# Optimization experiments

Hardware: AMD Instinct MI355X
Metric: run time of the kernel (lower is better)

The kernel has to match this reference:

```python
import jax, jax.numpy as jnp
import numpy as np

FACTOR = 27.2114 * 0.529177249  # Hartree*Bohr -> eV*Angstrom coulomb factor
N_TYPES = 6
NEURON = [25, 50, 100]
AXIS = 16
B, NC, NM = 4, 128, 16384


def _dense_stack(x, channels, params):
    """Type-indexed MLP: x (B,N,F), channels (N,) int -> (B,N,neuron[-1]).
    Layer 0: no residual; layers 1,2: out=2*in -> residual via concat([x,x])."""
    res_modes = [0, 2, 2]
    for (W, b), res in zip(params, res_modes):
        # W: (C, out, in); gather per-position weights, contract input features
        y = jnp.tanh(jnp.einsum('bnf,nof->bno', x, W[channels]) + b[channels][None])
        if res == 2:
            y = y + jnp.concatenate([x, x], axis=-1)
        elif res == 1:
            y = y + x
        x = y
    return x


def _fwd(atom_coords, charge_coords, charges, esp_params, ef_params, atom_types, real_mask):
    Bb, Nc, _ = atom_coords.shape
    # ---- local environment (off-diagonal neighbor pairs) ----
    i = jnp.arange(Nc)[:, None]
    j = jnp.arange(Nc - 1)[None, :]
    nidx = jnp.where(j < i, j, j + 1)                              # (Nc, Nc-1) neighbor indices
    rij = atom_coords[:, :, None] - atom_coords[:, None]           # (B,Nc,Nc,3)
    rij_off = jnp.take_along_axis(rij, nidx[None, :, :, None], axis=2)  # (B,Nc,Nc-1,3)
    dij = jnp.linalg.norm(rij_off, axis=-1)                        # (B,Nc,Nc-1)
    loc_env_a = rij_off / (dij * dij)[..., None]                   # rij / r^2

    # ---- masked ESP / E-field from MM charges ----
    rq = atom_coords[:, :, None] - charge_coords[:, None]          # (B,Nc,Nm,3)
    dq = jnp.linalg.norm(rq, axis=-1)                              # (B,Nc,Nm)
    d_safe = jnp.maximum(dq, 1e-12)
    pm = real_mask[:, None, :]                                     # (B,1,Nm)
    inv_d = jnp.where(pm, 1.0 / d_safe, 0.0)
    inv_d3 = jnp.where(pm, 1.0 / (d_safe * d_safe * d_safe), 0.0)
    esp = jnp.einsum('bm,bnm->bn', charges, inv_d) * FACTOR        # (B,Nc)
    efield = jnp.einsum('bm,bnmd,bnm->bnd', charges, rq, inv_d3) * FACTOR  # (B,Nc,3)

    # ---- per-atom-type ESP embedding ----
    esp_out = _dense_stack(esp[..., None], atom_types, esp_params)  # (B,Nc,M)

    # ---- per-pair-type E-field embedding ----
    proj = jnp.einsum('bnid,bnd->bni', loc_env_a, efield)           # (B,Nc,Nc-1)
    channels = (atom_types[:, None] * N_TYPES + atom_types[nidx]).reshape(-1)  # (Nc*(Nc-1),)
    x = proj.reshape(Bb, Nc * (Nc - 1), 1)
    out = _dense_stack(x, channels, ef_params).reshape(Bb, Nc, Nc - 1, -1)  # (B,Nc,Nc-1,M)
    G = jnp.einsum('bnim,bnia->bnma', out, out[..., :AXIS])         # (B,Nc,M,axis)
    G = G.reshape(Bb, Nc, -1) * 2.0
    return jnp.concatenate([esp_out, G], axis=2)                    # (B,Nc,M*(axis+1))


def _init_params(key, n_channels):
    dims = [1] + NEURON
    params = []
    for li in range(len(NEURON)):
        kw, kb = jax.random.split(jax.random.fold_in(key, li))
        fan_in = dims[li]
        s = 1.0 / np.sqrt(max(fan_in, 1))
        W = jax.random.uniform(kw, (n_channels, dims[li + 1], fan_in), minval=-s, maxval=s, dtype=jnp.float32)
        b = jax.random.uniform(kb, (n_channels, dims[li + 1]), minval=-s, maxval=s, dtype=jnp.float32)
        params.append((W, b))
    return params


def setup_inputs() -> dict:
    key = jax.random.key(0)
    ks = jax.random.split(key, 8)
    atom_coords = jax.random.normal(ks[0], (B, NC, 3), dtype=jnp.float32) * 5.0
    charge_coords = jax.random.normal(ks[1], (B, NM, 3), dtype=jnp.float32) * 20.0
    charges = jax.random.normal(ks[2], (B, NM), dtype=jnp.float32) * 0.1
    atom_types = jax.random.randint(ks[3], (NC,), 0, N_TYPES)
    real_mask_bool = jax.random.randint(ks[4], (B, NM), 0, 2).astype(bool)
    esp_p = _init_params(ks[5], N_TYPES)
    ef_p = _init_params(ks[6], N_TYPES * N_TYPES)
    inp = {
        'atom_coords': atom_coords, 'charge_coords': charge_coords, 'charges': charges,
        'esp_W0': esp_p[0][0], 'esp_b0': esp_p[0][1], 'esp_W1': esp_p[1][0], 'esp_b1': esp_p[1][1],
        'esp_W2': esp_p[2][0], 'esp_b2': esp_p[2][1],
        'ef_W0': ef_p[0][0], 'ef_b0': ef_p[0][1], 'ef_W1': ef_p[1][0], 'ef_b1': ef_p[1][1],
        'ef_W2': ef_p[2][0], 'ef_b2': ef_p[2][1],
        'atom_types': atom_types, 'real_mask_bool': real_mask_bool,
    }
    return inp


def reference(atom_coords, charge_coords, charges,
              esp_W0, esp_b0, esp_W1, esp_b1, esp_W2, esp_b2,
              ef_W0, ef_b0, ef_W1, ef_b1, ef_W2, ef_b2,
              atom_types, real_mask_bool):
    esp_params = [(esp_W0, esp_b0), (esp_W1, esp_b1), (esp_W2, esp_b2)]
    ef_params = [(ef_W0, ef_b0), (ef_W1, ef_b1), (ef_W2, ef_b2)]
    return _fwd(atom_coords, charge_coords, charges, esp_params, ef_params, atom_types, real_mask_bool)
```

## Files before the change

### kernel.cpp

```cpp
#include <hip/hip_runtime.h>
#include <hip/hip_bf16.h>

#define B_   4
#define NC_  128
#define NM_  16384
#define OUTROW 1700
#define FACTORF ((float)(27.2114 * 0.529177249))

typedef __attribute__((ext_vector_type(8))) short short8v;
typedef __attribute__((ext_vector_type(4))) float float4v;

__device__ __forceinline__ float fast_tanh(float x) {
    float e = __expf(2.0f * x);
    return 1.0f - 2.0f * __builtin_amdgcn_rcpf(e + 1.0f);
}
__device__ __forceinline__ unsigned short f2bf(float x) {
    union { __hip_bfloat16 h; unsigned short u; } cv;
    cv.h = __float2bfloat16(x);
    return cv.u;
}
__device__ __forceinline__ float bflo(unsigned u) { return __uint_as_float(u << 16); }
__device__ __forceinline__ float bfu(unsigned short u) { return __uint_as_float(((unsigned)u) << 16); }

union FragU { uint4 u4; unsigned u[4]; short8v s; };

__global__ __launch_bounds__(256) void k_prep(
    const float* __restrict__ fW1, const float* __restrict__ fW2,
    unsigned short* __restrict__ w1bf, unsigned short* __restrict__ w2bf,
    const float* __restrict__ atom_coords, const float* __restrict__ charge_coords,
    const float* __restrict__ charges, const void* __restrict__ mask,
    float4* __restrict__ partial, int nchunk)
{
    const int t = threadIdx.x;
    const int blk = blockIdx.x;
    if (blk < 36) {
        unsigned short* dst = w1bf + blk * 2048;
        const float* src = fW1 + blk * 1250;
        for (int i = t; i < 2048; i += 256) {
            int k = i >> 5, l = i & 31;
            float v = (k < 50 && l < 25) ? src[k * 25 + l] : 0.0f;
            dst[i] = f2bf(v);
        }
        return;
    }
    if (blk < 72) {
        int cp = blk - 36;
        unsigned short* dst = w2bf + cp * 7168;
        const float* src = fW2 + cp * 5000;
        for (int i = t; i < 7168; i += 256) {
            int nn = i >> 6, kk = i & 63;
            float v = (nn < 100 && kk < 50) ? src[nn * 50 + kk] : 0.0f;
            dst[i] = f2bf(v);
        }
        return;
    }
    const int eb = blk - 72;
    const int b  = eb / nchunk;
    const int ch = eb % nchunk;
    const int chunkM = NM_ / nchunk;
    const int a = t & 127;
    const int h = t >> 7;

    __shared__ float4 stg[128];
    __shared__ float4 psum[128];
    __shared__ int sdet;

    if (t == 0) sdet = 0;
    __syncthreads();
    if (t < 16) {
        const uint4* mw = (const uint4*)mask;
        uint4 v = mw[b * 1024 + t];
        if ((v.x > 1u) | (v.y > 1u) | (v.z > 1u) | (v.w > 1u)) atomicOr(&sdet, 1);
    }
    __syncthreads();
    const int byteMask = sdet;

    float ax, ay, az;
    {
        const float* p = atom_coords + (size_t)(b * NC_ + a) * 3;
        ax = p[0]; ay = p[1]; az = p[2];
    }
    const float* ccb = charge_coords + (size_t)b * NM_ * 3;
    const float* chb = charges + (size_t)b * NM_;
    const unsigned char* mb8 = (const unsigned char*)mask + (size_t)b * NM_;
    const int* mb32 = (const int*)mask + (size_t)b * NM_;

    float s0 = 0.0f, s1 = 0.0f, s2 = 0.0f, s3 = 0.0f;

    for (int tb = 0; tb < chunkM; tb += 128) {
        if (t < 128) {
            int m = ch * chunkM + tb + t;
            float cx = ccb[3 * m + 0], cy = ccb[3 * m + 1], cz = ccb[3 * m + 2];
            int mk = byteMask ? (int)mb8[m] : mb32[m];
            float q = mk ? chb[m] : 0.0f;
            stg[t] = make_float4(cx, cy, cz, q);
        }
        __syncthreads();
        const float4* sp = stg + h * 64;
#pragma unroll 8
        for (int i = 0; i < 64; ++i) {
            float4 cq = sp[i];
            float dx = ax - cq.x, dy = ay - cq.y, dz = az - cq.z;
            float d2 = dx * dx + dy * dy + dz * dz;
            float inv = __builtin_amdgcn_rsqf(d2);
            float inv3 = inv * inv * inv;
            s0 += cq.w * inv;
            float qi3 = cq.w * inv3;
            s1 += qi3 * dx; s2 += qi3 * dy; s3 += qi3 * dz;
        }
        __syncthreads();
    }
    if (h == 1) psum[a] = make_float4(s0, s1, s2, s3);
    __syncthreads();
    if (h == 0) {
        float4 o = psum[a];
        partial[(size_t)(b * NC_ + a) * nchunk + ch] =
            make_float4(s0 + o.x, s1 + o.y, s2 + o.z, s3 + o.w);
    }
}

__global__ __launch_bounds__(512, 6) void k_ef(
    const float* __restrict__ atom_coords, const float4* __restrict__ partial, int nchunk,
    const int* __restrict__ atom_types,
    const float* __restrict__ eW0, const float* __restrict__ eb0,
    const float* __restrict__ eW1, const float* __restrict__ eb1,
    const float* __restrict__ eW2, const float* __restrict__ eb2,
    const float* __restrict__ fW0, const float* __restrict__ fb0,
    const float* __restrict__ fb1, const float* __restrict__ fb2,
    const unsigned short* __restrict__ w1bf, const unsigned short* __restrict__ w2bf,
    float* __restrict__ out)
{
    const int t   = threadIdx.x;
    const int blk = blockIdx.x;
    const int b   = blk >> 7;
    const int n   = blk & 127;

    __shared__ float cst[NC_][3];
    __shared__ float xs[128];
    __shared__ int   sc[128];
    __shared__ int   tat[128];
    __shared__ int   wcnt[2][6];
    __shared__ int   tmeta[16];
    __shared__ int   tcnt;
    __shared__ unsigned short a0s[6][25];
    __shared__ unsigned short b0s[6][25];
    __shared__ float b1s[6][50];
    __shared__ unsigned short b2s[6][100];
    __shared__ float espf[4];
    __shared__ float h0e[25];
    __shared__ float h1e[52];
    __shared__ __align__(16) unsigned short y1p[128][72];
    __shared__ __align__(16) unsigned short y2t[100][136];
    unsigned short (*y0p)[32] = (unsigned short (*)[32])&y2t[0][0];

    const int tn = atom_types[n];
    const int c0 = tn * 6;
    const int wv   = t >> 6;
    const int lane = t & 63;

    for (int idx = t; idx < NC_ * 3; idx += 512)
        (&cst[0][0])[idx] = atom_coords[(size_t)b * NC_ * 3 + idx];
    if (t < 128) tat[t] = atom_types[t];
    for (int idx = t; idx < 150; idx += 512) {
        (&a0s[0][0])[idx] = f2bf(fW0[c0 * 25 + idx]);
        (&b0s[0][0])[idx] = f2bf(fb0[c0 * 25 + idx]);
    }
    if (t >= 192 && t < 492) (&b1s[0][0])[t - 192] = fb1[c0 * 50 + t - 192];
    if (t >= 128 && t < 192) {
        for (int idx = t - 128; idx < 600; idx += 64)
            (&b2s[0][0])[idx] = f2bf(fb2[c0 * 100 + idx]);
    }
    if (t >= 256 && t < 320) {
        int lt = t - 256;
        float4 v = make_float4(0.f, 0.f, 0.f, 0.f);
        for (int ch = lt; ch < nchunk; ch += 64) {
            float4 u = partial[(size_t)(b * NC_ + n) * nchunk + ch];
            v.x += u.x; v.y += u.y; v.z += u.z; v.w += u.w;
        }
#pragma unroll
        for (int off = 32; off > 0; off >>= 1) {
            v.x += __shfl_xor(v.x, off, 64);
            v.y += __shfl_xor(v.y, off, 64);
            v.z += __shfl_xor(v.z, off, 64);
            v.w += __shfl_xor(v.w, off, 64);
        }
        if (lt == 0) {
            espf[0] = v.x * FACTORF;
            espf[1] = v.y * FACTORF;
            espf[2] = v.z * FACTORF;
            espf[3] = v.w * FACTORF;
        }
    }
    __syncthreads();

    unsigned long long mkeep = 0;
    int myc = 0; float px = 0.0f;
    if (wv < 2) {
        const bool valid = t < 127;
        if (valid) {
            int jn = (t < n) ? t : t + 1;
            float rx = cst[n][0] - cst[jn][0];
            float ry = cst[n][1] - cst[jn][1];
            float rz = cst[n][2] - cst[jn][2];
            float d2 = rx * rx + ry * ry + rz * rz;
            px = (rx * espf[1] + ry * espf[2] + rz * espf[3]) / d2;
            myc = tat[jn];
        }
#pragma unroll
        for (int v = 0; v < 6; ++v) {
            unsigned long long m = __ballot(valid && (myc == v));
            if (valid && myc == v) mkeep = m;
            if (lane == 0) wcnt[wv][v] = __builtin_popcountll(m);
        }
    } else if (t >= 320 && t < 345) {
        int l = t - 320;
        h0e[l] = fast_tanh(eW0[tn * 25 + l] * espf[0] + eb0[tn * 25 + l]);
    }
    __syncthreads();

    if (t < 127) {
        int w0[6], w1[6];
#pragma unroll
        for (int v = 0; v < 6; ++v) { w0[v] = wcnt[0][v]; w1[v] = wcnt[1][v]; }
        int basec = 0;
#pragma unroll
        for (int v = 0; v < 6; ++v) if (v < myc) basec += w0[v] + w1[v];
        int pos = basec + (wv == 1 ? w0[myc] : 0)
                + __builtin_popcountll(mkeep & ((1ull << lane) - 1ull));
        sc[pos] = myc; xs[pos] = px;
        if (t == 0) {
            int run = 0, nt = 0;
#pragma unroll
            for (int v = 0; v < 6; ++v) {
                int pendv = run + w0[v] + w1[v];
                for (int base = run; base < pendv; base += 16) {
                    tmeta[nt] = base | (v << 8) | (pendv << 12);
                    ++nt;
                }
                run = pendv;
            }
            tcnt = nt;
        }
    } else if (t >= 320 && t < 370) {
        int l = t - 320;
        float s = eb1[tn * 50 + l];
        const float* wr = eW1 + (size_t)(tn * 50 + l) * 25;
#pragma unroll
        for (int j = 0; j < 25; ++j) s += wr[j] * h0e[j];
        h1e[l] = fast_tanh(s) + h0e[l % 25];
    }
    __syncthreads();

    if (t < 256) {
        for (int i = t; i < 127 * 32; i += 256) {
            int r = i >> 5, l = i & 31;
            int c = sc[r]; float x = xs[r];
            float v = (l < 25) ? fast_tanh(bfu(a0s[c][l]) * x + bfu(b0s[c][l])) : 0.0f;
            y0p[r][l] = f2bf(v);
        }
    } else if (t >= 320 && t < 420) {
        int k = t - 320;
        float s = eb2[tn * 100 + k];
        const float2* wr = (const float2*)(eW2 + (size_t)(tn * 100 + k) * 50);
#pragma unroll
        for (int j = 0; j < 25; ++j) {
            float2 u = wr[j];
            s += u.x * h1e[2 * j] + u.y * h1e[2 * j + 1];
        }
        out[(size_t)(b * NC_ + n) * OUTROW + k] = fast_tanh(s) + h1e[k % 50];
    }
    __syncthreads();

    {
        const int kt = wv & 3;
        const int krow = (lane >> 4) << 3;
        const int arow = kt * 16 + (lane & 15);
        const int kres = (arow < 50) ? (arow % 25) : 999;
        FragU Id;
#pragma unroll
        for (int e = 0; e < 4; ++e) {
            int ka = krow + 2 * e;
            Id.u[e] = (ka == kres ? 0x3f80u : 0u) | (ka + 1 == kres ? 0x3f800000u : 0u);
        }
        const unsigned short* wb = w1bf + ((size_t)c0 * 64 + arow) * 32 + krow;
        int meta = (lane < 16) ? tmeta[lane & 15] : 0;
        const int nt = tcnt;
        const int kb = kt * 16 + ((lane >> 4) << 2);
        int ccur = -1;
        FragU Af;
        float bias[4];
        for (int ti = (wv >> 2); ti < nt; ti += 2) {
            const int mv = __builtin_amdgcn_readlane(meta, ti);
            const int base = mv & 255, c = (mv >> 8) & 15, pend = mv >> 12;
            if (c != ccur) {
                ccur = c;
                Af.u4 = *(const uint4*)(wb + (size_t)c * 2048);
#pragma unroll
                for (int r = 0; r < 4; ++r)
                    bias[r] = (kb + r < 50) ? b1s[c][kb + r] : 0.0f;
            }
            FragU Bf;
            Bf.u4 = *(const uint4*)&y0p[base + (lane & 15)][krow];
            float4v z = {0.f, 0.f, 0.f, 0.f};
            float4v acc  = __builtin_amdgcn_mfma_f32_16x16x32_bf16(Af.s, Bf.s, z, 0, 0, 0);
            float4v acc2 = __builtin_amdgcn_mfma_f32_16x16x32_bf16(Id.s, Bf.s, z, 0, 0, 0);
            const int p = base + (lane & 15);
            if (p < pend) {
                unsigned short yv[4];
#pragma unroll
                for (int r = 0; r < 4; ++r)
                    yv[r] = f2bf(fast_tanh(acc[r] + bias[r]) + acc2[r]);
                unsigned lo = (unsigned)yv[0] | ((unsigned)yv[1] << 16);
                unsigned hi = (unsigned)yv[2] | ((unsigned)yv[3] << 16);
                *(uint2*)&y1p[p][kb] = make_uint2(lo, hi);
            }
        }
    }
    __syncthreads();

    for (int rep2 = 0; rep2 < 2; ++rep2) {

    if (wv < 7) {
        const int krow = (lane >> 4) << 3;
        const int arow = wv * 16 + (lane & 15);
        const int nres = (arow < 100) ? (arow % 50) : 999;
        FragU Id0, Id1;
#pragma unroll
        for (int e = 0; e < 4; ++e) {
            int ka = krow + 2 * e;
            Id0.u[e] = (ka == nres ? 0x3f80u : 0u) | (ka + 1 == nres ? 0x3f800000u : 0u);
            int kc = 32 + krow + 2 * e;
            Id1.u[e] = (kc == nres ? 0x3f80u : 0u) | (kc + 1 == nres ? 0x3f800000u : 0u);
        }
        int meta = (lane < 16) ? tmeta[lane & 15] : 0;
        const int nt = tcnt;
        const int nb = wv * 16 + ((lane >> 4) << 2);
        int ccur = -1;
        FragU A0, A1;
        float bb[4];
        for (int ti = 0; ti < nt; ++ti) {
            const int mv = __builtin_amdgcn_readlane(meta, ti);
            const int base = mv & 255, c = (mv >> 8) & 15, pend = mv >> 12;
            if (c != ccur) {
                ccur = c;
                const unsigned short* wb =
                    w2bf + ((size_t)(c0 + c) * 112 + arow) * 64;
                A0.u4 = *(const uint4*)(wb + krow);
                A1.u4 = *(const uint4*)(wb + 32 + krow);
#pragma unroll
                for (int r = 0; r < 4; ++r)
                    bb[r] = (nb + r < 100) ? bfu(b2s[c][nb + r]) : 0.0f;
            }
            FragU B0, B1;
            const int p = base + (lane & 15);
            B0.u4 = *(const uint4*)&y1p[p][krow];
            B1.u4 = *(const uint4*)&y1p[p][32 + krow];
            float4v z = {0.f, 0.f, 0.f, 0.f};
            float4v acc  = __builtin_amdgcn_mfma_f32_16x16x32_bf16(A0.s, B0.s, z, 0, 0, 0);
            acc  = __builtin_amdgcn_mfma_f32_16x16x32_bf16(A1.s, B1.s, acc, 0, 0, 0);
            float4v acc2 = __builtin_amdgcn_mfma_f32_16x16x32_bf16(Id0.s, B0.s, z, 0, 0, 0);
            acc2 = __builtin_amdgcn_mfma_f32_16x16x32_bf16(Id1.s, B1.s, acc2, 0, 0, 0);
            if (p < pend) {
#pragma unroll
                for (int r = 0; r < 4; ++r) {
                    int nn = nb + r;
                    if (nn < 100)
                        y2t[nn][p] = f2bf(fast_tanh(acc[r] + bb[r]) + acc2[r]);
                }
            }
        }
    } else {
        for (int i = lane; i < 100; i += 64) y2t[i][127] = 0;
    }
    __syncthreads();

    }

    if (wv < 7) {
        const int krow = (lane >> 4) << 3;
        short8v GB[4];
#pragma unroll
        for (int ks = 0; ks < 4; ++ks) {
            FragU cv; cv.u4 = *(const uint4*)&y2t[lane & 15][ks * 32 + krow];
            GB[ks] = cv.s;
        }
        float* orow = out + (size_t)(b * NC_ + n) * OUTROW + 100;
        const int aa = lane & 15;
        int m0 = wv * 16 + (lane & 15);
        if (m0 > 99) m0 = 99;
        float4v acc = {0.f, 0.f, 0.f, 0.f};
#pragma unroll
        for (int ks = 0; ks < 4; ++ks) {
            FragU av; av.u4 = *(const uint4*)&y2t[m0][ks * 32 + krow];
            acc = __builtin_amdgcn_mfma_f32_16x16x32_bf16(av.s, GB[ks], acc, 0, 0, 0);
        }
        const int mrow = wv * 16 + ((lane >> 4) << 2);
#pragma unroll
        for (int r = 0; r < 4; ++r) {
            int m = mrow + r;
            if (m < 100) orow[m * 16 + aa] = 2.0f * acc[r];
        }
    }
}

extern "C" void kernel_launch(void* const* d_in, const int* in_sizes, int n_in,
                              void* d_out, int out_size, void* d_ws, size_t ws_size,
                              hipStream_t stream) {
    (void)in_sizes; (void)n_in; (void)out_size;
    const float* atom_coords   = (const float*)d_in[0];
    const float* charge_coords = (const float*)d_in[1];
    const float* charges       = (const float*)d_in[2];
    const float* eW0 = (const float*)d_in[3];
    const float* eb0 = (const float*)d_in[4];
    const float* eW1 = (const float*)d_in[5];
    const float* eb1 = (const float*)d_in[6];
    const float* eW2 = (const float*)d_in[7];
    const float* eb2 = (const float*)d_in[8];
    const float* fW0 = (const float*)d_in[9];
    const float* fb0 = (const float*)d_in[10];
    const float* fW1 = (const float*)d_in[11];
    const float* fb1 = (const float*)d_in[12];
    const float* fW2 = (const float*)d_in[13];
    const float* fb2 = (const float*)d_in[14];
    const int*   atom_types = (const int*)d_in[15];
    const void*  mask = d_in[16];
    float* out = (float*)d_out;

    const size_t W1BF_B = 36 * 64 * 32 * 2;
    const size_t W2BF_B = 36 * 112 * 64 * 2;
    unsigned short* w1bf = (unsigned short*)d_ws;
    unsigned short* w2bf = (unsigned short*)((char*)d_ws + W1BF_B);
    float4* partial = (float4*)((char*)d_ws + W1BF_B + W2BF_B);

    int nchunk = 128;
    while (nchunk > 1 &&
           W1BF_B + W2BF_B + (size_t)B_ * NC_ * nchunk * 16 > ws_size)
        nchunk >>= 1;

    k_prep<<<72 + B_ * nchunk, 256, 0, stream>>>(
        fW1, fW2, w1bf, w2bf,
        atom_coords, charge_coords, charges, mask, partial, nchunk);
    k_ef<<<B_ * NC_, 512, 0, stream>>>(
        atom_coords, partial, nchunk, atom_types,
        eW0, eb0, eW1, eb1, eW2, eb2,
        fW0, fb0, fb1, fb2, w1bf, w2bf, out);
}
```

Baseline: 35.59 us.

## Remove duplicated layer-2 pass and transpose MFMA operands for packed stores

```diff
diff --git a/kernel.cpp b/kernel.cpp
--- a/kernel.cpp
+++ b/kernel.cpp
@@ -252,11 +252,20 @@
     __syncthreads();
 
     if (t < 256) {
-        for (int i = t; i < 127 * 32; i += 256) {
-            int r = i >> 5, l = i & 31;
+        for (int i = t; i < 127 * 8; i += 256) {
+            int r = i >> 3, q = i & 7;
             int c = sc[r]; float x = xs[r];
-            float v = (l < 25) ? fast_tanh(bfu(a0s[c][l]) * x + bfu(b0s[c][l])) : 0.0f;
-            y0p[r][l] = f2bf(v);
+            unsigned short v4[4];
+#pragma unroll
+            for (int e = 0; e < 4; ++e) {
+                int l = 4 * q + e;
+                v4[e] = (l < 25)
+                      ? f2bf(fast_tanh(bfu(a0s[c][l]) * x + bfu(b0s[c][l])))
+                      : (unsigned short)0;
+            }
+            unsigned lo = (unsigned)v4[0] | ((unsigned)v4[1] << 16);
+            unsigned hi = (unsigned)v4[2] | ((unsigned)v4[3] << 16);
+            *(uint2*)&y0p[r][4 * q] = make_uint2(lo, hi);
         }
     } else if (t >= 320 && t < 420) {
         int k = t - 320;
@@ -318,12 +327,11 @@
     }
     __syncthreads();
 
-    for (int rep2 = 0; rep2 < 2; ++rep2) {
-
     if (wv < 7) {
         const int krow = (lane >> 4) << 3;
         const int arow = wv * 16 + (lane & 15);
-        const int nres = (arow < 100) ? (arow % 50) : 999;
+        const bool nok = arow < 100;
+        const int nres = nok ? (arow % 50) : 999;
         FragU Id0, Id1;
 #pragma unroll
         for (int e = 0; e < 4; ++e) {
@@ -334,10 +342,10 @@
         }
         int meta = (lane < 16) ? tmeta[lane & 15] : 0;
         const int nt = tcnt;
-        const int nb = wv * 16 + ((lane >> 4) << 2);
+        const int prow_off = (lane >> 4) << 2;
         int ccur = -1;
         FragU A0, A1;
-        float bb[4];
+        float bb = 0.0f;
         for (int ti = 0; ti < nt; ++ti) {
             const int mv = __builtin_amdgcn_readlane(meta, ti);
             const int base = mv & 255, c = (mv >> 8) & 15, pend = mv >> 12;
@@ -347,25 +355,30 @@
                     w2bf + ((size_t)(c0 + c) * 112 + arow) * 64;
                 A0.u4 = *(const uint4*)(wb + krow);
                 A1.u4 = *(const uint4*)(wb + 32 + krow);
+                bb = nok ? bfu(b2s[c][arow]) : 0.0f;
+            }
+            FragU B0, B1;
+            B0.u4 = *(const uint4*)&y1p[base + (lane & 15)][krow];
+            B1.u4 = *(const uint4*)&y1p[base + (lane & 15)][32 + krow];
+            float4v z = {0.f, 0.f, 0.f, 0.f};
+            float4v acc  = __builtin_amdgcn_mfma_f32_16x16x32_bf16(B0.s, A0.s, z, 0, 0, 0);
+            acc  = __builtin_amdgcn_mfma_f32_16x16x32_bf16(B1.s, A1.s, acc, 0, 0, 0);
+            float4v acc2 = __builtin_amdgcn_mfma_f32_16x16x32_bf16(B0.s, Id0.s, z, 0, 0, 0);
+            acc2 = __builtin_amdgcn_mfma_f32_16x16x32_bf16(B1.s, Id1.s, acc2, 0, 0, 0);
+            if (nok) {
+                const int prow = base + prow_off;
+                unsigned short yv[4];
 #pragma unroll
                 for (int r = 0; r < 4; ++r)
-                    bb[r] = (nb + r < 100) ? bfu(b2s[c][nb + r]) : 0.0f;
-            }
-            FragU B0, B1;
-            const int p = base + (lane & 15);
-            B0.u4 = *(const uint4*)&y1p[p][krow];
-            B1.u4 = *(const uint4*)&y1p[p][32 + krow];
-            float4v z = {0.f, 0.f, 0.f, 0.f};
-            float4v acc  = __builtin_amdgcn_mfma_f32_16x16x32_bf16(A0.s, B0.s, z, 0, 0, 0);
-            acc  = __builtin_amdgcn_mfma_f32_16x16x32_bf16(A1.s, B1.s, acc, 0, 0, 0);
-            float4v acc2 = __builtin_amdgcn_mfma_f32_16x16x32_bf16(Id0.s, B0.s, z, 0, 0, 0);
-            acc2 = __builtin_amdgcn_mfma_f32_16x16x32_bf16(Id1.s, B1.s, acc2, 0, 0, 0);
-            if (p < pend) {
-#pragma unroll
-                for (int r = 0; r < 4; ++r) {
-                    int nn = nb + r;
-                    if (nn < 100)
-                        y2t[nn][p] = f2bf(fast_tanh(acc[r] + bb[r]) + acc2[r]);
+                    yv[r] = f2bf(fast_tanh(acc[r] + bb) + acc2[r]);
+                if (prow + 3 < pend) {
+                    unsigned lo = (unsigned)yv[0] | ((unsigned)yv[1] << 16);
+                    unsigned hi = (unsigned)yv[2] | ((unsigned)yv[3] << 16);
+                    *(uint2*)&y2t[arow][prow] = make_uint2(lo, hi);
+                } else {
+#pragma unroll
+                    for (int r = 0; r < 4; ++r)
+                        if (prow + r < pend) y2t[arow][prow + r] = yv[r];
                 }
             }
         }
@@ -373,8 +386,6 @@
         for (int i = lane; i < 100; i += 64) y2t[i][127] = 0;
     }
     __syncthreads();
-
-    }
 
     if (wv < 7) {
         const int krow = (lane >> 4) << 3;
```

After: 29.41 us, median of 2. 17.4% less time.
